# Optimization experiments

Measured on AMD Instinct MI355X. Metric: run time of the kernel, lower is better.

## Reference

```python
import jax, jax.numpy as jnp
import numpy as np

B, NQ, NKV = 2, 1024, 4096
DQ = 1024          # query_dim == context_dim
H, DH = 16, 64     # heads, dim_head
INNER = H * DH     # 1024
SCALE = DH ** -0.5


def setup_inputs() -> dict:
    key = jax.random.key(0)
    ks = jax.random.split(key, 6)
    s = 1.0 / np.sqrt(DQ)
    return {
        "x": jax.random.normal(ks[0], (B, NQ, DQ), dtype=jnp.float32),
        "context": jax.random.normal(ks[1], (B, NKV, DQ), dtype=jnp.float32),
        "Wq": jax.random.normal(ks[2], (DQ, INNER), dtype=jnp.float32) * s,
        "Wkv": jax.random.normal(ks[3], (DQ, 2 * INNER), dtype=jnp.float32) * s,
        "Wout": jax.random.normal(ks[4], (INNER, DQ), dtype=jnp.float32) * (1.0 / np.sqrt(INNER)),
        "b_out": jax.random.normal(ks[5], (DQ,), dtype=jnp.float32) * 0.01,
    }


def _split_heads(t):
    # b n (h d) -> b h n d
    b, n, _ = t.shape
    return t.reshape(b, n, H, DH).transpose(0, 2, 1, 3)


def reference(x, context, Wq, Wkv, Wout, b_out):
    q = x @ Wq                       # [B, NQ, INNER]
    kv = context @ Wkv               # [B, NKV, 2*INNER]
    k, v = jnp.split(kv, 2, axis=-1)
    q, k, v = map(_split_heads, (q, k, v))          # [B, H, n, DH]
    sim = jnp.einsum("bhid,bhjd->bhij", q, k) * SCALE  # [B, H, NQ, NKV]
    attn = jax.nn.softmax(sim, axis=-1)
    out = jnp.einsum("bhij,bhjd->bhid", attn, v)       # [B, H, NQ, DH]
    out = out.transpose(0, 2, 1, 3).reshape(B, NQ, INNER)  # (b h) n d -> b n (h d)
    return out @ Wout + b_out
```

## Files before the change

kernel.cpp:

```cpp
#include <hip/hip_runtime.h>
#include <stdint.h>

#define B_    2
#define NQ_   1024
#define NKV_  4096
#define DQ_   1024
#define H_    16
#define DH_   64
#define INNER_ 1024

typedef unsigned short u16;
typedef uint32_t u32;
typedef __bf16 bf16x8 __attribute__((ext_vector_type(8)));
typedef float  f32x4  __attribute__((ext_vector_type(4)));

__device__ __forceinline__ u16 f2bf(float x) {
  union { float f; uint32_t u; } v; v.f = x;
  uint32_t r = v.u + 0x7FFFu + ((v.u >> 16) & 1u);
  return (u16)(r >> 16);
}
__device__ __forceinline__ u32 pack2(float a, float b) {
  return (u32)f2bf(a) | ((u32)f2bf(b) << 16);
}
__device__ __forceinline__ u32 pack2rn(float a, float b) {
  union { float f; u32 u; } x, y; x.f = a; y.f = b;
  return __builtin_amdgcn_perm(y.u + 0x8000u, x.u + 0x8000u, 0x07060302u);
}
__device__ __forceinline__ float bf2f(u16 s) {
  union { float f; uint32_t u; } v; v.u = ((uint32_t)s) << 16; return v.f;
}

__device__ __forceinline__ void gload16(const void* g, void* l) {
  __builtin_amdgcn_global_load_lds((const __attribute__((address_space(1))) void*)g,
                                   (__attribute__((address_space(3))) void*)l,
                                   16, 0, 0);
}

__global__ __launch_bounds__(256) void prep(const float* __restrict__ x,
                                            const float* __restrict__ ctx,
                                            const float* __restrict__ Wq,
                                            const float* __restrict__ Wkv,
                                            const float* __restrict__ Wout,
                                            u16* __restrict__ xb,
                                            u16* __restrict__ ctxb,
                                            u16* __restrict__ WqT,
                                            u16* __restrict__ WkvT,
                                            u16* __restrict__ WoutT) {
  int bid = blockIdx.x;
  if (bid < 1280) {
    const float* src; u16* dst; int fbase;
    if (bid < 256) { src = x;   dst = xb;   fbase = bid * 2048; }
    else           { src = ctx; dst = ctxb; fbase = (bid - 256) * 2048; }
#pragma unroll
    for (int u = 0; u < 8; ++u) {
      int i = (fbase + u * 256 + threadIdx.x) * 4;
      float4 v = *(const float4*)(src + i);
      uint2 o; o.x = pack2(v.x, v.y); o.y = pack2(v.z, v.w);
      *(uint2*)(dst + i) = o;
    }
    return;
  }
  __shared__ float tile[32][33];
  const float* W; u16* Wt; int K, N, local, nsh;
  int b2 = bid - 1280;
  if (b2 < 1024)      { W = Wq;   Wt = WqT;   K = 1024; N = 1024; local = b2;        nsh = 5; }
  else if (b2 < 3072) { W = Wkv;  Wt = WkvT;  K = 1024; N = 2048; local = b2 - 1024; nsh = 6; }
  else                { W = Wout; Wt = WoutT; K = 1024; N = 1024; local = b2 - 3072; nsh = 5; }
  int n0 = (local & ((1 << nsh) - 1)) * 32;
  int k0 = (local >> nsh) * 32;
  int tx = threadIdx.x & 31, ty = threadIdx.x >> 5;
  for (int i = ty; i < 32; i += 8)
    tile[i][tx] = W[(size_t)(k0 + i) * N + n0 + tx];
  __syncthreads();
  for (int i = ty; i < 32; i += 8)
    Wt[(size_t)(n0 + i) * K + k0 + tx] = f2bf(tile[tx][i]);
}

__global__ __launch_bounds__(512, 2) void kv_gemm(const u16* __restrict__ ctxb,
                                                  const u16* __restrict__ WkvT,
                                                  u16* __restrict__ kb,
                                                  u16* __restrict__ vTb) {
  __shared__ __align__(16) u16 As[2][256 * 64];
  __shared__ __align__(16) u16 Bs[2][256 * 64];
  const int tid = threadIdx.x;
  const int lane = tid & 63;
  const int w = tid >> 6;
  const int wr = w >> 2, wc = w & 3;
  const int l15 = lane & 15, quad = lane >> 4;
  const int K = 1024;

  int bid = blockIdx.x;
  int wgid = (bid & 7) * 32 + (bid >> 3);
  const int tm = wgid >> 3, tn = wgid & 7;
  const int m0 = tm * 256, n0 = tn * 256;
  const u16* Ag = ctxb + (size_t)m0 * K;
  const u16* Bg = WkvT + (size_t)n0 * K;

  size_t offA[2][2], offB[2][2];
#pragma unroll
  for (int ah = 0; ah < 2; ++ah)
#pragma unroll
    for (int p = 0; p < 2; ++p) {
      int c = p * 512 + (w << 6) + lane;
      int s = ah * 128 + (c >> 3);
      int col = ((c & 7) ^ (s & 7)) << 3;
      int rA = ((s >> 6) & 1) * 128 + ((s >> 7) & 1) * 64 + (s & 63);
      int rB = ((s >> 5) & 3) * 64 + ((s >> 7) & 1) * 32 + (s & 31);
      offA[ah][p] = (size_t)rA * 1024 + col;
      offB[ah][p] = (size_t)rB * 1024 + col;
    }

#define STAGE_A(bufi, ah, kk) do { \
    gload16(Ag + offA[ah][0] + (kk), &As[bufi][(ah) * 8192 + (w << 9)]); \
    gload16(Ag + offA[ah][1] + (kk), &As[bufi][(ah) * 8192 + 4096 + (w << 9)]); \
  } while (0)
#define STAGE_B(bufi, bh, kk) do { \
    gload16(Bg + offB[bh][0] + (kk), &Bs[bufi][(bh) * 8192 + (w << 9)]); \
    gload16(Bg + offB[bh][1] + (kk), &Bs[bufi][(bh) * 8192 + 4096 + (w << 9)]); \
  } while (0)
#define LDA2(dst, i8, bufi) do { \
    const int _s = ((i8) >> 2) * 128 + wr * 64 + ((i8) & 3) * 16 + l15; \
    const u16* _p = &As[bufi][_s * 64]; const int _x = _s & 7; \
    dst[0] = *(const bf16x8*)&_p[(quad ^ _x) << 3]; \
    dst[1] = *(const bf16x8*)&_p[((quad + 4) ^ _x) << 3]; \
  } while (0)
#define LDB2(dst, j, bufi) do { \
    const int _s = ((j) >> 1) * 128 + wc * 32 + ((j) & 1) * 16 + l15; \
    const u16* _p = &Bs[bufi][_s * 64]; const int _x = _s & 7; \
    dst[0] = *(const bf16x8*)&_p[(quad ^ _x) << 3]; \
    dst[1] = *(const bf16x8*)&_p[((quad + 4) ^ _x) << 3]; \
  } while (0)
#define MF(i0, j0, bb) do { \
    _Pragma("unroll") \
    for (int _i = 0; _i < 4; ++_i) { \
      acc[(i0) + _i][(j0)    ] = __builtin_amdgcn_mfma_f32_16x16x32_bf16(a[_i][0], bb[0][0], acc[(i0) + _i][(j0)    ], 0, 0, 0); \
      acc[(i0) + _i][(j0)    ] = __builtin_amdgcn_mfma_f32_16x16x32_bf16(a[_i][1], bb[0][1], acc[(i0) + _i][(j0)    ], 0, 0, 0); \
      acc[(i0) + _i][(j0) + 1] = __builtin_amdgcn_mfma_f32_16x16x32_bf16(a[_i][0], bb[1][0], acc[(i0) + _i][(j0) + 1], 0, 0, 0); \
      acc[(i0) + _i][(j0) + 1] = __builtin_amdgcn_mfma_f32_16x16x32_bf16(a[_i][1], bb[1][1], acc[(i0) + _i][(j0) + 1], 0, 0, 0); \
    } \
  } while (0)
#define BAR()   __builtin_amdgcn_s_barrier()
#define LGKM0() asm volatile("s_waitcnt lgkmcnt(0)" ::: "memory")

  f32x4 acc[8][4] = {};
  bf16x8 a[4][2], b[2][2], c2[2][2];

  STAGE_A(0, 0, 0);
  STAGE_B(0, 0, 0);
  STAGE_B(0, 1, 0);
  STAGE_A(0, 1, 0);
  STAGE_A(1, 0, 64);
  STAGE_B(1, 0, 64);
  STAGE_B(1, 1, 64);
  asm volatile("s_waitcnt vmcnt(6)" ::: "memory");
  BAR();

#define HALF(bufi, kAb, kNext, STG, WMID, WEND) do { \
     \
    LDB2(b[0], 0, bufi); LDB2(b[1], 1, bufi); \
    LDA2(a[0], 0, bufi); LDA2(a[1], 1, bufi); LDA2(a[2], 2, bufi); LDA2(a[3], 3, bufi); \
    if (kAb >= 0) STAGE_A((bufi) ^ 1, 1, kAb); \
    BAR(); LGKM0(); \
    __builtin_amdgcn_s_setprio(1); MF(0, 0, b); __builtin_amdgcn_s_setprio(0); \
    BAR(); \
     \
    LDB2(c2[0], 2, bufi); LDB2(c2[1], 3, bufi); \
    if (STG) STAGE_A(bufi, 0, kNext); \
    BAR(); LGKM0(); \
    __builtin_amdgcn_s_setprio(1); MF(0, 2, c2); __builtin_amdgcn_s_setprio(0); \
    BAR(); \
     \
    LDA2(a[0], 4, bufi); LDA2(a[1], 5, bufi); LDA2(a[2], 6, bufi); LDA2(a[3], 7, bufi); \
    if (STG) STAGE_B(bufi, 0, kNext); \
    BAR(); LGKM0(); \
    __builtin_amdgcn_s_setprio(1); MF(4, 0, b); __builtin_amdgcn_s_setprio(0); \
    BAR(); \
     \
    if (STG) STAGE_B(bufi, 1, kNext); \
    BAR(); \
    __builtin_amdgcn_s_setprio(1); MF(4, 2, c2); __builtin_amdgcn_s_setprio(0); \
    WMID; \
    BAR(); \
  } while (0)

  for (int i = 0; i < 7; ++i) {
    const int k2 = i * 128;
    HALF(0, k2 + 64, k2 + 128, 1,
         asm volatile("s_waitcnt vmcnt(6)" ::: "memory"), );
    HALF(1, k2 + 128, k2 + 192, 1,
         asm volatile("s_waitcnt vmcnt(6)" ::: "memory"), );
  }
  HALF(0, 960, 0, 0,
       asm volatile("s_waitcnt vmcnt(0)" ::: "memory"), );
  HALF(1, -1, 0, 0, , );

#undef HALF
#undef BAR
#undef LGKM0

  if (tn < 4) {
#pragma unroll
    for (int i8 = 0; i8 < 8; ++i8)
#pragma unroll
      for (int j = 0; j < 4; ++j) {
        int col = n0 + wc * 64 + j * 16 + l15;
#pragma unroll
        for (int r = 0; r < 4; ++r) {
          int row = m0 + wr * 128 + i8 * 16 + quad * 4 + r;
          kb[(size_t)row * 1024 + col] = f2bf(acc[i8][j][r]);
        }
      }
  } else {
    const int bb_ = m0 >> 12;
#pragma unroll
    for (int i8 = 0; i8 < 8; ++i8) {
      int kvr = (m0 & 4095) + wr * 128 + i8 * 16 + quad * 4;
#pragma unroll
      for (int j = 0; j < 4; ++j) {
        int c = (n0 - 1024) + wc * 64 + j * 16 + l15;
        int h = c >> 6, dh = c & 63;
        uint2 st;
        st.x = pack2(acc[i8][j][0], acc[i8][j][1]);
        st.y = pack2(acc[i8][j][2], acc[i8][j][3]);
        *(uint2*)&vTb[((size_t)((bb_ * 16 + h) * 64 + dh)) * NKV_ + kvr] = st;
      }
    }
  }
#undef STAGE_A
#undef STAGE_B
#undef LDA2
#undef LDB2
#undef MF
}

__global__ __launch_bounds__(256) void q_gemm(const u16* __restrict__ A,
                                              const u16* __restrict__ Bt,
                                              u16* __restrict__ outp) {
  __shared__ __align__(16) u16 As[64 * 32];
  __shared__ __align__(16) u16 Bs[128 * 32];
  const int tid = threadIdx.x;
  const int lane = tid & 63;
  const int w = tid >> 6;
  const int wr = w >> 1, wc = w & 1;
  const int l15 = lane & 15, quad = lane >> 4;
  const int unit = blockIdx.x;
  const int m0 = (unit >> 3) * 64, n0 = (unit & 7) * 128;
  const int K = 1024, N = 1024;

  const u16* Ab = A + (size_t)m0 * K;
  const u16* Bb = Bt + (size_t)n0 * K;
  f32x4 acc[2][4] = {};

  const int ar = tid >> 2, ac = (tid & 3) << 3;
  const int q1 = w * 64 + lane, q2 = q1 + 256;
  const int br1 = q1 >> 2, bc1 = (q1 & 3) << 3;
  const int br2 = q2 >> 2, bc2 = (q2 & 3) << 3;

  for (int k0 = 0; k0 < K; k0 += 32) {
    __syncthreads();
    gload16(Ab + (size_t)ar * K + k0 + ac, &As[w * 512]);
    gload16(Bb + (size_t)br1 * K + k0 + bc1, &Bs[w * 512]);
    gload16(Bb + (size_t)br2 * K + k0 + bc2, &Bs[2048 + w * 512]);
    __syncthreads();
    bf16x8 af[2], bfr[4];
#pragma unroll
    for (int i = 0; i < 2; ++i)
      af[i] = *(const bf16x8*)&As[(wr * 32 + i * 16 + l15) * 32 + quad * 8];
#pragma unroll
    for (int j = 0; j < 4; ++j)
      bfr[j] = *(const bf16x8*)&Bs[(wc * 64 + j * 16 + l15) * 32 + quad * 8];
#pragma unroll
    for (int i = 0; i < 2; ++i)
#pragma unroll
      for (int j = 0; j < 4; ++j)
        acc[i][j] = __builtin_amdgcn_mfma_f32_16x16x32_bf16(af[i], bfr[j], acc[i][j], 0, 0, 0);
  }

#pragma unroll
  for (int i = 0; i < 2; ++i)
#pragma unroll
    for (int j = 0; j < 4; ++j) {
      int col = n0 + wc * 64 + j * 16 + l15;
#pragma unroll
      for (int r = 0; r < 4; ++r) {
        int row = m0 + wr * 32 + i * 16 + quad * 4 + r;
        outp[(size_t)row * N + col] = f2bf(acc[i][j][r]);
      }
    }
}

__global__ __launch_bounds__(256) void out_gemm(const u16* __restrict__ A,
                                                const u16* __restrict__ Bt,
                                                float* __restrict__ Cout,
                                                const float* __restrict__ bias) {
  __shared__ __align__(16) u16 As[64 * 32];
  __shared__ __align__(16) u16 Bs[128 * 32];
  const int tid = threadIdx.x;
  const int lane = tid & 63;
  const int w = tid >> 6;
  const int wr = w >> 1, wc = w & 1;
  const int l15 = lane & 15, quad = lane >> 4;
  const int unit = blockIdx.x;
  const int m0 = (unit >> 3) * 64, n0 = (unit & 7) * 128;
  const int K = 1024, N = 1024;

  const u16* Ab = A + (size_t)m0 * K;
  const u16* Bb = Bt + (size_t)n0 * K;
  f32x4 acc[2][4] = {};

  const int ar = tid >> 2, ac = (tid & 3) << 3;
  const int q1 = w * 64 + lane, q2 = q1 + 256;
  const int br1 = q1 >> 2, bc1 = (q1 & 3) << 3;
  const int br2 = q2 >> 2, bc2 = (q2 & 3) << 3;

  for (int k0 = 0; k0 < K; k0 += 32) {
    __syncthreads();
    gload16(Ab + (size_t)ar * K + k0 + ac, &As[w * 512]);
    gload16(Bb + (size_t)br1 * K + k0 + bc1, &Bs[w * 512]);
    gload16(Bb + (size_t)br2 * K + k0 + bc2, &Bs[2048 + w * 512]);
    __syncthreads();
    bf16x8 af[2], bfr[4];
#pragma unroll
    for (int i = 0; i < 2; ++i)
      af[i] = *(const bf16x8*)&As[(wr * 32 + i * 16 + l15) * 32 + quad * 8];
#pragma unroll
    for (int j = 0; j < 4; ++j)
      bfr[j] = *(const bf16x8*)&Bs[(wc * 64 + j * 16 + l15) * 32 + quad * 8];
#pragma unroll
    for (int i = 0; i < 2; ++i)
#pragma unroll
      for (int j = 0; j < 4; ++j)
        acc[i][j] = __builtin_amdgcn_mfma_f32_16x16x32_bf16(af[i], bfr[j], acc[i][j], 0, 0, 0);
  }

#pragma unroll
  for (int i = 0; i < 2; ++i)
#pragma unroll
    for (int j = 0; j < 4; ++j) {
      int col = n0 + wc * 64 + j * 16 + l15;
      float bv = bias[col];
#pragma unroll
      for (int r = 0; r < 4; ++r) {
        int row = m0 + wr * 32 + i * 16 + quad * 4 + r;
        Cout[(size_t)row * N + col] = acc[i][j][r] + bv;
      }
    }
}

__global__ __launch_bounds__(256, 2) void attn_kernel(const u16* __restrict__ qg,
                                                      const u16* __restrict__ kb,
                                                      const u16* __restrict__ vT,
                                                      u16* __restrict__ attn_out) {
  __shared__ __align__(16) u16 Ks[128 * 64];
  __shared__ __align__(16) u16 Vs[64 * 128];
  __shared__ __align__(16) u32 P32[4 * 4 * 16 * 20];
  __shared__ float Lr[4][4][16];

  const int tid = threadIdx.x;
  const int lane = tid & 63;
  const int w = tid >> 6;
  const int l15 = lane & 15, quad = lane >> 4;
  const int bh = blockIdx.x, b = bh >> 4, h = bh & 15;
  const int q0 = blockIdx.y * 64;

  const float SC = 0.125f * 1.44269504088896340736f;
  union { u16 s[8]; bf16x8 v; } qf[4][2];
#pragma unroll
  for (int t = 0; t < 4; ++t)
#pragma unroll
    for (int kc = 0; kc < 2; ++kc) {
      const u16* qp = qg + (size_t)(b * NQ_ + q0 + t * 16 + l15) * INNER_ + h * 64 +
                      kc * 32 + quad * 8;
      union { u16 s[8]; uint4 u; } tmp;
      tmp.u = *(const uint4*)qp;
#pragma unroll
      for (int e = 0; e < 8; ++e) qf[t][kc].s[e] = f2bf(bf2f(tmp.s[e]) * SC);
    }

#define STAGEKV(j0) do { \
    _Pragma("unroll") \
    for (int i_ = 0; i_ < 4; ++i_) { \
      int s_ = i_ * 256 + tid; \
      int kr = s_ >> 3, kg = (s_ ^ kr) & 7; \
      gload16(kb + (size_t)(b * NKV_ + (j0) + kr) * 1024 + h * 64 + kg * 8, \
              &Ks[(i_ * 256 + w * 64) * 8]); \
      int vr = s_ >> 4, vg = (s_ ^ vr) & 15; \
      gload16(vT + (size_t)(bh * 64 + vr) * NKV_ + (j0) + vg * 8, \
              &Vs[(i_ * 256 + w * 64) * 8]); \
    } \
  } while (0)

  f32x4 Oacc[4][4] = {};
  float l_lane[4] = {0.f, 0.f, 0.f, 0.f};

  STAGEKV(0);

  for (int it = 0; it < 32; ++it) {
    __syncthreads();

    bf16x8 kf[2][2];
#pragma unroll
    for (int kvt = 0; kvt < 2; ++kvt)
#pragma unroll
      for (int kc = 0; kc < 2; ++kc)
        kf[kvt][kc] = *(const bf16x8*)
          &Ks[(w * 32 + kvt * 16 + l15) * 64 + (((kc * 4 + quad) ^ l15) & 7) * 8];
    bf16x8 vf[4];
#pragma unroll
    for (int d = 0; d < 4; ++d)
      vf[d] = *(const bf16x8*)
        &Vs[(d * 16 + l15) * 128 + (((w * 4 + quad) ^ l15) & 15) * 8];

    __syncthreads();

    if (it < 31) STAGEKV((it + 1) * 128);

    f32x4 sacc[2][4] = {};
    __builtin_amdgcn_s_setprio(1);
#pragma unroll
    for (int kvt = 0; kvt < 2; ++kvt)
#pragma unroll
      for (int t = 0; t < 4; ++t)
#pragma unroll
        for (int kc = 0; kc < 2; ++kc)
          sacc[kvt][t] = __builtin_amdgcn_mfma_f32_16x16x32_bf16(
              kf[kvt][kc], qf[t][kc].v, sacc[kvt][t], 0, 0, 0);
    __builtin_amdgcn_s_setprio(0);

#pragma unroll
    for (int kvt = 0; kvt < 2; ++kvt)
#pragma unroll
      for (int t = 0; t < 4; ++t) {
        float p0 = __builtin_amdgcn_exp2f(sacc[kvt][t][0]);
        float p1 = __builtin_amdgcn_exp2f(sacc[kvt][t][1]);
        float p2 = __builtin_amdgcn_exp2f(sacc[kvt][t][2]);
        float p3 = __builtin_amdgcn_exp2f(sacc[kvt][t][3]);
        l_lane[t] += (p0 + p1) + (p2 + p3);
        uint2 pk; pk.x = pack2rn(p0, p1); pk.y = pack2rn(p2, p3);
        *(uint2*)&P32[((w * 4 + t) * 16 + l15) * 20 + kvt * 8 + quad * 2] = pk;
      }

    bf16x8 pf[4];
#pragma unroll
    for (int t = 0; t < 4; ++t)
      pf[t] = *(const bf16x8*)&P32[((w * 4 + t) * 16 + l15) * 20 + quad * 4];
    __builtin_amdgcn_s_setprio(1);
#pragma unroll
    for (int d = 0; d < 4; ++d)
#pragma unroll
      for (int t = 0; t < 4; ++t)
        Oacc[d][t] = __builtin_amdgcn_mfma_f32_16x16x32_bf16(vf[d], pf[t], Oacc[d][t],
                                                             0, 0, 0);
    __builtin_amdgcn_s_setprio(0);
  }
#undef STAGEKV

#pragma unroll
  for (int t = 0; t < 4; ++t) {
    l_lane[t] += __shfl_xor(l_lane[t], 16);
    l_lane[t] += __shfl_xor(l_lane[t], 32);
  }
  if (quad == 0) {
#pragma unroll
    for (int t = 0; t < 4; ++t) Lr[w][t][l15] = l_lane[t];
  }
  __syncthreads();
  float inv = 1.0f / (Lr[0][w][l15] + Lr[1][w][l15] + Lr[2][w][l15] + Lr[3][w][l15]);

  float* red = (float*)P32;
  u16* ob = attn_out + (size_t)(b * NQ_ + q0 + w * 16 + l15) * INNER_ + h * 64;
#pragma unroll
  for (int d = 0; d < 4; ++d) {
    __syncthreads();
#pragma unroll
    for (int t = 0; t < 4; ++t)
      *(f32x4*)&red[(w * 4 + t) * 256 + quad * 64 + l15 * 4] = Oacc[d][t];
    __syncthreads();
    f32x4 r = *(const f32x4*)&red[(0 * 4 + w) * 256 + quad * 64 + l15 * 4];
#pragma unroll
    for (int ww = 1; ww < 4; ++ww) {
      f32x4 c = *(const f32x4*)&red[(ww * 4 + w) * 256 + quad * 64 + l15 * 4];
      r[0] += c[0]; r[1] += c[1]; r[2] += c[2]; r[3] += c[3];
    }
    *(u32*)(ob + d * 16 + quad * 4)     = pack2(r[0] * inv, r[1] * inv);
    *(u32*)(ob + d * 16 + quad * 4 + 2) = pack2(r[2] * inv, r[3] * inv);
  }
}

extern "C" void kernel_launch(void* const* d_in, const int* in_sizes, int n_in,
                              void* d_out, int out_size, void* d_ws, size_t ws_size,
                              hipStream_t stream) {
  const float* x    = (const float*)d_in[0];
  const float* ctx  = (const float*)d_in[1];
  const float* Wq   = (const float*)d_in[2];
  const float* Wkv  = (const float*)d_in[3];
  const float* Wout = (const float*)d_in[4];
  const float* bout = (const float*)d_in[5];

  char* ws = (char*)d_ws;
  u16* xb    = (u16*)(ws + (size_t)( 0u << 20));
  u16* ab    = (u16*)(ws + (size_t)( 0u << 20));
  u16* ctxb  = (u16*)(ws + (size_t)( 4u << 20));
  u16* WqT   = (u16*)(ws + (size_t)(20u << 20));
  u16* WkvT  = (u16*)(ws + (size_t)(22u << 20));
  u16* WoutT = (u16*)(ws + (size_t)(26u << 20));
  u16* qb    = (u16*)(ws + (size_t)(28u << 20));
  u16* kb    = (u16*)(ws + (size_t)(32u << 20));
  u16* vTb   = (u16*)(ws + (size_t)(48u << 20));

  prep<<<5376, 256, 0, stream>>>(x, ctx, Wq, Wkv, Wout, xb, ctxb, WqT, WkvT, WoutT);
  q_gemm<<<256, 256, 0, stream>>>(xb, WqT, qb);
  kv_gemm<<<256, 512, 0, stream>>>(ctxb, WkvT, kb, vTb);
  attn_kernel<<<dim3(32, 16), 256, 0, stream>>>(qb, kb, vTb, ab);
  out_gemm<<<256, 256, 0, stream>>>(ab, WoutT, (float*)d_out, bout);
}
```

Measured before the change: 221.5 us.

## Fuse Q projection GEMM into attention kernel prologue

Removes the separate q_gemm launch. Each attention block now computes its own 64x64 Q tile (x rows times one head's Wq slice) with MFMA, staging through the K/V shared buffers with XOR swizzling before the softmax loop. This saves one kernel launch and the round trip of Q through global memory. In exchange, every attention block runs a K=1024 GEMM prologue with a simple single-buffered load loop. The ab buffer moves so it no longer aliases xb, which is still read during attention.

```diff
diff --git a/kernel.cpp b/kernel.cpp
--- a/kernel.cpp
+++ b/kernel.cpp
@@ -156,26 +156,22 @@
   BAR();
 
 #define HALF(bufi, kAb, kNext, STG, WMID, WEND) do { \
-     \
     LDB2(b[0], 0, bufi); LDB2(b[1], 1, bufi); \
     LDA2(a[0], 0, bufi); LDA2(a[1], 1, bufi); LDA2(a[2], 2, bufi); LDA2(a[3], 3, bufi); \
     if (kAb >= 0) STAGE_A((bufi) ^ 1, 1, kAb); \
     BAR(); LGKM0(); \
     __builtin_amdgcn_s_setprio(1); MF(0, 0, b); __builtin_amdgcn_s_setprio(0); \
     BAR(); \
-     \
     LDB2(c2[0], 2, bufi); LDB2(c2[1], 3, bufi); \
     if (STG) STAGE_A(bufi, 0, kNext); \
     BAR(); LGKM0(); \
     __builtin_amdgcn_s_setprio(1); MF(0, 2, c2); __builtin_amdgcn_s_setprio(0); \
     BAR(); \
-     \
     LDA2(a[0], 4, bufi); LDA2(a[1], 5, bufi); LDA2(a[2], 6, bufi); LDA2(a[3], 7, bufi); \
     if (STG) STAGE_B(bufi, 0, kNext); \
     BAR(); LGKM0(); \
     __builtin_amdgcn_s_setprio(1); MF(4, 0, b); __builtin_amdgcn_s_setprio(0); \
     BAR(); \
-     \
     if (STG) STAGE_B(bufi, 1, kNext); \
     BAR(); \
     __builtin_amdgcn_s_setprio(1); MF(4, 2, c2); __builtin_amdgcn_s_setprio(0); \
@@ -231,62 +227,6 @@
 #undef LDA2
 #undef LDB2
 #undef MF
-}
-
-__global__ __launch_bounds__(256) void q_gemm(const u16* __restrict__ A,
-                                              const u16* __restrict__ Bt,
-                                              u16* __restrict__ outp) {
-  __shared__ __align__(16) u16 As[64 * 32];
-  __shared__ __align__(16) u16 Bs[128 * 32];
-  const int tid = threadIdx.x;
-  const int lane = tid & 63;
-  const int w = tid >> 6;
-  const int wr = w >> 1, wc = w & 1;
-  const int l15 = lane & 15, quad = lane >> 4;
-  const int unit = blockIdx.x;
-  const int m0 = (unit >> 3) * 64, n0 = (unit & 7) * 128;
-  const int K = 1024, N = 1024;
-
-  const u16* Ab = A + (size_t)m0 * K;
-  const u16* Bb = Bt + (size_t)n0 * K;
-  f32x4 acc[2][4] = {};
-
-  const int ar = tid >> 2, ac = (tid & 3) << 3;
-  const int q1 = w * 64 + lane, q2 = q1 + 256;
-  const int br1 = q1 >> 2, bc1 = (q1 & 3) << 3;
-  const int br2 = q2 >> 2, bc2 = (q2 & 3) << 3;
-
-  for (int k0 = 0; k0 < K; k0 += 32) {
-    __syncthreads();
-    gload16(Ab + (size_t)ar * K + k0 + ac, &As[w * 512]);
-    gload16(Bb + (size_t)br1 * K + k0 + bc1, &Bs[w * 512]);
-    gload16(Bb + (size_t)br2 * K + k0 + bc2, &Bs[2048 + w * 512]);
-    __syncthreads();
-    bf16x8 af[2], bfr[4];
-#pragma unroll
-    for (int i = 0; i < 2; ++i)
-      af[i] = *(const bf16x8*)&As[(wr * 32 + i * 16 + l15) * 32 + quad * 8];
-#pragma unroll
-    for (int j = 0; j < 4; ++j)
-      bfr[j] = *(const bf16x8*)&Bs[(wc * 64 + j * 16 + l15) * 32 + quad * 8];
-#pragma unroll
-    for (int i = 0; i < 2; ++i)
-#pragma unroll
-      for (int j = 0; j < 4; ++j)
-        acc[i][j] = __builtin_amdgcn_mfma_f32_16x16x32_bf16(af[i], bfr[j], acc[i][j], 0, 0, 0);
-  }
-
-#pragma unroll
-  for (int i = 0; i < 2; ++i)
-#pragma unroll
-    for (int j = 0; j < 4; ++j) {
-      int col = n0 + wc * 64 + j * 16 + l15;
-#pragma unroll
-      for (int r = 0; r < 4; ++r) {
-        int row = m0 + wr * 32 + i * 16 + quad * 4 + r;
-        outp[(size_t)row * N + col] = f2bf(acc[i][j][r]);
-      }
-    }
 }
 
 __global__ __launch_bounds__(256) void out_gemm(const u16* __restrict__ A,
@@ -347,7 +287,8 @@
     }
 }
 
-__global__ __launch_bounds__(256, 2) void attn_kernel(const u16* __restrict__ qg,
+__global__ __launch_bounds__(256, 2) void attn_kernel(const u16* __restrict__ xb,
+                                                      const u16* __restrict__ WqT,
                                                       const u16* __restrict__ kb,
                                                       const u16* __restrict__ vT,
                                                       u16* __restrict__ attn_out) {
@@ -365,17 +306,63 @@
 
   const float SC = 0.125f * 1.44269504088896340736f;
   union { u16 s[8]; bf16x8 v; } qf[4][2];
-#pragma unroll
-  for (int t = 0; t < 4; ++t)
-#pragma unroll
-    for (int kc = 0; kc < 2; ++kc) {
-      const u16* qp = qg + (size_t)(b * NQ_ + q0 + t * 16 + l15) * INNER_ + h * 64 +
-                      kc * 32 + quad * 8;
-      union { u16 s[8]; uint4 u; } tmp;
-      tmp.u = *(const uint4*)qp;
-#pragma unroll
-      for (int e = 0; e < 8; ++e) qf[t][kc].s[e] = f2bf(bf2f(tmp.s[e]) * SC);
+
+  {
+    const u16* Axb = xb + (size_t)(b * NQ_ + q0) * 1024;
+    const u16* Bwq = WqT + (size_t)(h * 64) * 1024;
+    const int c1 = tid, c2 = tid + 256;
+    const int r1 = c1 >> 3, g1 = c1 & 7;
+    const int r2 = c2 >> 3, g2 = c2 & 7;
+    const size_t sO1 = (size_t)r1 * 1024 + (size_t)((g1 ^ (r1 & 7)) << 3);
+    const size_t sO2 = (size_t)r2 * 1024 + (size_t)((g2 ^ (r2 & 7)) << 3);
+    f32x4 qacc[4] = {};
+    const int x7 = l15 & 7;
+    for (int k0 = 0; k0 < 1024; k0 += 64) {
+      __syncthreads();
+      gload16(Axb + sO1 + k0, &Ks[w * 512]);
+      gload16(Axb + sO2 + k0, &Ks[2048 + w * 512]);
+      gload16(Bwq + sO1 + k0, &Ks[4096 + w * 512]);
+      gload16(Bwq + sO2 + k0, &Ks[6144 + w * 512]);
+      __syncthreads();
+      bf16x8 af[2], bfr[4][2];
+#pragma unroll
+      for (int kc = 0; kc < 2; ++kc) {
+        af[kc] = *(const bf16x8*)&Ks[(w * 16 + l15) * 64 + (((kc * 4 + quad) ^ x7) << 3)];
+#pragma unroll
+        for (int j = 0; j < 4; ++j)
+          bfr[j][kc] = *(const bf16x8*)
+            &Ks[4096 + (j * 16 + l15) * 64 + (((kc * 4 + quad) ^ x7) << 3)];
+      }
+#pragma unroll
+      for (int j = 0; j < 4; ++j) {
+        qacc[j] = __builtin_amdgcn_mfma_f32_16x16x32_bf16(af[0], bfr[j][0], qacc[j], 0, 0, 0);
+        qacc[j] = __builtin_amdgcn_mfma_f32_16x16x32_bf16(af[1], bfr[j][1], qacc[j], 0, 0, 0);
+      }
     }
+    float* Q64 = (float*)Vs;
+#pragma unroll
+    for (int j = 0; j < 4; ++j)
+#pragma unroll
+      for (int r = 0; r < 4; ++r) {
+        int row = w * 16 + quad * 4 + r;
+        Q64[row * 64 + ((j * 16 + l15) ^ ((row & 7) * 8))] = qacc[j][r];
+      }
+    __syncthreads();
+#pragma unroll
+    for (int t = 0; t < 4; ++t)
+#pragma unroll
+      for (int kc = 0; kc < 2; ++kc) {
+        const float* qp = Q64 + (t * 16 + l15) * 64 + (((kc * 4 + quad) ^ x7) * 8);
+        f32x4 lo = *(const f32x4*)qp;
+        f32x4 hi = *(const f32x4*)(qp + 4);
+#pragma unroll
+        for (int e = 0; e < 4; ++e) {
+          qf[t][kc].s[e]     = f2bf(lo[e] * SC);
+          qf[t][kc].s[e + 4] = f2bf(hi[e] * SC);
+        }
+      }
+    __syncthreads();
+  }
 
 #define STAGEKV(j0) do { \
     _Pragma("unroll") \
@@ -499,18 +486,16 @@
 
   char* ws = (char*)d_ws;
   u16* xb    = (u16*)(ws + (size_t)( 0u << 20));
-  u16* ab    = (u16*)(ws + (size_t)( 0u << 20));
   u16* ctxb  = (u16*)(ws + (size_t)( 4u << 20));
   u16* WqT   = (u16*)(ws + (size_t)(20u << 20));
   u16* WkvT  = (u16*)(ws + (size_t)(22u << 20));
   u16* WoutT = (u16*)(ws + (size_t)(26u << 20));
-  u16* qb    = (u16*)(ws + (size_t)(28u << 20));
+  u16* ab    = (u16*)(ws + (size_t)(28u << 20));
   u16* kb    = (u16*)(ws + (size_t)(32u << 20));
   u16* vTb   = (u16*)(ws + (size_t)(48u << 20));
 
   prep<<<5376, 256, 0, stream>>>(x, ctx, Wq, Wkv, Wout, xb, ctxb, WqT, WkvT, WoutT);
-  q_gemm<<<256, 256, 0, stream>>>(xb, WqT, qb);
   kv_gemm<<<256, 512, 0, stream>>>(ctxb, WkvT, kb, vTb);
-  attn_kernel<<<dim3(32, 16), 256, 0, stream>>>(qb, kb, vTb, ab);
+  attn_kernel<<<dim3(32, 16), 256, 0, stream>>>(xb, WqT, kb, vTb, ab);
   out_gemm<<<256, 256, 0, stream>>>(ab, WoutT, (float*)d_out, bout);
 }
```

Result: faster. 213.5 us (-3.6%).
